# Performance work log

Measured on AMD Instinct MI355X. Metric: run time of the kernel, lower is better.

The kernel has to match this reference:

```python
import jax, jax.numpy as jnp
import numpy as np

N, E, IN, H, C, OUT = 50000, 800000, 128, 4, 32, 40
HID = H * C  # 128


def _layernorm(x, g, b, eps=1e-5):
    mu = x.mean(-1, keepdims=True)
    var = ((x - mu) ** 2).mean(-1, keepdims=True)
    return (x - mu) * jax.lax.rsqrt(var + eps) * g + b


def _gatv2(x, src, dst, Wl, bl, Wr, br, att, bias, heads, ch, concat):
    n = x.shape[0]
    xl = (x @ Wl + bl).reshape(n, heads, ch)  # source-side transform
    xr = (x @ Wr + br).reshape(n, heads, ch)  # target-side transform
    e = jax.nn.leaky_relu(xl[src] + xr[dst], 0.2)          # [E,H,C]
    alpha = jnp.einsum('ehc,hc->eh', e, att)                # [E,H]
    m = jax.ops.segment_max(alpha, dst, num_segments=n)
    m = jnp.where(jnp.isfinite(m), m, 0.0)
    a = jnp.exp(alpha - m[dst])
    denom = jax.ops.segment_sum(a, dst, num_segments=n)
    a = a / (denom[dst] + 1e-16)
    out = jax.ops.segment_sum(xl[src] * a[:, :, None], dst, num_segments=n)  # [N,H,C]
    out = out.reshape(n, heads * ch) if concat else out.mean(1)
    return out + bias


def setup_inputs():
    key = jax.random.key(0)
    ks = jax.random.split(key, 26)
    s = 0.05
    rn = lambda k, sh: jax.random.normal(k, sh, jnp.float32) * s
    inp = {
        'x': jax.random.normal(ks[0], (N, IN), jnp.float32),
        'edge_index': jax.random.randint(ks[1], (2, E), 0, N, jnp.int64),
        'W0': rn(ks[2], (IN, HID)), 'b0': jnp.zeros((HID,), jnp.float32),
        'W1l': rn(ks[3], (IN, HID)), 'b1l': jnp.zeros((HID,), jnp.float32),
        'W1r': rn(ks[4], (IN, HID)), 'b1r': jnp.zeros((HID,), jnp.float32),
        'att1': rn(ks[5], (H, C)), 'bias1': jnp.zeros((HID,), jnp.float32),
        'g1': jnp.ones((HID,), jnp.float32), 'be1': jnp.zeros((HID,), jnp.float32),
        'W2l': rn(ks[6], (HID, HID)), 'b2l': jnp.zeros((HID,), jnp.float32),
        'W2r': rn(ks[7], (HID, HID)), 'b2r': jnp.zeros((HID,), jnp.float32),
        'att2': rn(ks[8], (H, C)), 'bias2': jnp.zeros((HID,), jnp.float32),
        'g2': jnp.ones((HID,), jnp.float32), 'be2': jnp.zeros((HID,), jnp.float32),
        'W3l': rn(ks[9], (HID, OUT)), 'b3l': jnp.zeros((OUT,), jnp.float32),
        'W3r': rn(ks[10], (HID, OUT)), 'b3r': jnp.zeros((OUT,), jnp.float32),
        'att3': rn(ks[11], (1, OUT)), 'bias3': jnp.zeros((OUT,), jnp.float32),
    }
    return inp


def reference(x, edge_index, W0, b0, W1l, b1l, W1r, b1r, att1, bias1, g1, be1,
              W2l, b2l, W2r, b2r, att2, bias2, g2, be2,
              W3l, b3l, W3r, b3r, att3, bias3):
    src, dst = edge_index[0], edge_index[1]
    identity = x @ W0 + b0
    out = _gatv2(x, src, dst, W1l, b1l, W1r, b1r, att1, bias1, H, C, True)
    out = jax.nn.gelu(_layernorm(out, g1, be1), approximate=False)
    x1 = out + identity  # dropout is identity in eval mode
    out = _gatv2(x1, src, dst, W2l, b2l, W2r, b2r, att2, bias2, H, C, True)
    out = jax.nn.gelu(_layernorm(out, g2, be2), approximate=False)
    x2 = out + x1
    return _gatv2(x2, src, dst, W3l, b3l, W3r, b3r, att3, bias3, 1, OUT, False)
```

## Files before the change

kernel.cpp:

```cpp
#include <hip/hip_runtime.h>
#include <hip/hip_bf16.h>

#define NN 50000
#define EE 800000
#define OUTD 40
#define NBUCK 196
#define BCAP 8192
#define ABLKS 200
#define EPB 4000

typedef __attribute__((ext_vector_type(8))) short short8;
typedef __attribute__((ext_vector_type(4))) float floatx4;

__device__ __forceinline__ float bf2f(unsigned short u) {
  union { unsigned int i; float f; } v; v.i = ((unsigned int)u) << 16; return v.f;
}
__device__ __forceinline__ unsigned short f2bf(float f) {
  union { float f; unsigned int i; } v; v.f = f;
  unsigned int x = v.i;
  return (unsigned short)((x + 0x7fffu + ((x >> 16) & 1u)) >> 16);
}
__device__ __forceinline__ float blo(unsigned int u) {
  union { unsigned int i; float f; } v; v.i = u << 16; return v.f;
}
__device__ __forceinline__ float bhi(unsigned int u) {
  union { unsigned int i; float f; } v; v.i = u & 0xffff0000u; return v.f;
}

template <int CTRL>
__device__ __forceinline__ float dpp_add(float x) {
  int y = __builtin_amdgcn_update_dpp(0, __float_as_int(x), CTRL, 0xF, 0xF, true);
  return x + __int_as_float(y);
}

__device__ __forceinline__ float gelu1(float y) {
  float y2 = y * y;
  float z = y * fmaf(0.0356774081f, y2, 0.7978845608f);
  float e = __expf(-2.f * z);
  float r = __builtin_amdgcn_rcpf(1.f + e);
  float th = fmaf(2.f, r, -1.f);
  return y * fmaf(0.5f, th, 0.5f);
}

__device__ __forceinline__ int probe_f32(const void* x) {
  int lane = threadIdx.x & 63;
  unsigned short u = ((const unsigned short*)x)[2 * lane];
  int exf = (u >> 7) & 0xFF;
  unsigned long long b = __ballot((exf >= 100 && exf <= 142) ? 1 : 0);
  return (__popcll(b) >= 48) ? 0 : 1;
}
__device__ __forceinline__ int probe_i64(const void* ei) {
  int lane = threadIdx.x & 63;
  long long v = ((const long long*)ei)[lane];
  unsigned long long b = __ballot((v >= 0 && v < NN) ? 1 : 0);
  return (__popcll(b) >= 48) ? 1 : 0;
}

struct WDesc { const void* W; unsigned short* F; int T; int ncols; };
struct WDescs { WDesc d[7]; int cum[8]; };
struct PCv { const void* s; unsigned short* d; int n; int cap; };
struct PCvs { PCv a[17]; };

__global__ __launch_bounds__(256) void init_kernel(const void* __restrict__ ei,
                                                   const void* __restrict__ x,
                                                   int* __restrict__ flags,
                                                   int* __restrict__ bcur,
                                                   WDescs ds, PCvs P) {
  int b = blockIdx.x;
  int f32 = probe_f32(x);
  if (b < 48) {
    int idx = b * 256 + threadIdx.x;
    if (idx >= 12288) return;
    int mi = 0;
    while (idx >= ds.cum[mi + 1]) mi++;
    int local = idx - ds.cum[mi];
    WDesc d = ds.d[mi];
    int lane = local & 63;
    int rest = local >> 6;
    int t = rest % d.T;
    int kb = rest / d.T;
    int m = lane & 15, quad = lane >> 4;
    int col = t * 16 + m;
    short8 v;
    for (int j = 0; j < 8; ++j) {
      int k = kb * 32 + quad * 8 + j;
      if (col < d.ncols) {
        int off = k * d.ncols + col;
        v[j] = f32 ? (short)f2bf(((const float*)d.W)[off])
                   : (short)((const unsigned short*)d.W)[off];
      } else {
        v[j] = 0;
      }
    }
    *(short8*)(d.F + (size_t)local * 8) = v;
  } else if (b < 65) {
    PCv p = P.a[b - 48];
    for (int i = threadIdx.x; i < p.cap; i += 256) {
      unsigned short o = 0;
      if (i < p.n)
        o = f32 ? f2bf(((const float*)p.s)[i]) : ((const unsigned short*)p.s)[i];
      p.d[i] = o;
    }
  } else {
    for (int i = threadIdx.x; i < NBUCK * 16; i += 256) bcur[i] = 0;
    if (threadIdx.x < 64) {
      int i64 = probe_i64(ei);
      if (threadIdx.x == 0) {
        flags[0] = i64;
        flags[1] = f32;
        flags[2] = 0;
      }
    }
  }
}

__global__ __launch_bounds__(256) void bucket_scatter_kernel(
    const void* __restrict__ ei, unsigned int* __restrict__ bedges,
    int* __restrict__ bcur) {
  __shared__ int lhist[NBUCK];
  __shared__ int lbase[NBUCK];
  int tid = threadIdx.x;
  if (tid < NBUCK) lhist[tid] = 0;
  int i64 = probe_i64(ei);
  __syncthreads();
  int e0 = blockIdx.x * EPB;
  int e1 = e0 + EPB; if (e1 > EE) e1 = EE;
  for (int e = e0 + tid; e < e1; e += 256) {
    int d = i64 ? (int)((const long long*)ei)[EE + e] : ((const int*)ei)[EE + e];
    d = d < 0 ? 0 : (d >= NN ? NN - 1 : d);
    atomicAdd(&lhist[d >> 8], 1);
  }
  __syncthreads();
  if (tid < NBUCK) {
    int c = lhist[tid];
    lbase[tid] = c ? atomicAdd(&bcur[tid * 16], c) : 0;
    lhist[tid] = 0;
  }
  __syncthreads();
  for (int e = e0 + tid; e < e1; e += 256) {
    int s, d;
    if (i64) {
      s = (int)((const long long*)ei)[e];
      d = (int)((const long long*)ei)[EE + e];
    } else {
      s = ((const int*)ei)[e];
      d = ((const int*)ei)[EE + e];
    }
    s = s < 0 ? 0 : (s >= NN ? NN - 1 : s);
    d = d < 0 ? 0 : (d >= NN ? NN - 1 : d);
    int bin = d >> 8;
    int r = atomicAdd(&lhist[bin], 1);
    int pos = lbase[bin] + r;
    if (pos < BCAP)
      bedges[(size_t)bin * BCAP + pos] =
          ((unsigned int)(d & 0xFF) << 24) | ((unsigned int)s << 8);
  }
}

__global__ __launch_bounds__(256) void bucket_sort_kernel(
    const unsigned int* __restrict__ bedges, const int* __restrict__ bcur,
    int* __restrict__ offs, int* __restrict__ src_sorted) {
  __shared__ int lhist[256];
  __shared__ int lscan[256];
  __shared__ int lbin[256];
  __shared__ int sbase, scount, stotal;
  __shared__ unsigned int le[BCAP];
  __shared__ unsigned short lrank[BCAP];
  int k = blockIdx.x;
  int tid = threadIdx.x;
  int c = 0;
  if (tid < NBUCK) {
    int v = bcur[tid * 16];
    c = v < BCAP ? v : BCAP;
  }
  lscan[tid] = c;
  __syncthreads();
  for (int off = 1; off < 256; off <<= 1) {
    int u = (tid >= off) ? lscan[tid - off] : 0;
    __syncthreads();
    lscan[tid] += u;
    __syncthreads();
  }
  if (tid == 0) {
    int pb = (k == 0) ? 0 : lscan[k - 1];
    sbase = pb;
    scount = lscan[k] - pb;
    stotal = lscan[NBUCK - 1];
  }
  lhist[tid] = 0;
  __syncthreads();
  int base = sbase, count = scount;
  const unsigned int* myb = bedges + (size_t)k * BCAP;
  for (int i = tid; i < count; i += 256) {
    unsigned int pk = myb[i];
    int bin = pk >> 24;
    int r = atomicAdd(&lhist[bin], 1);
    le[i] = pk;
    lrank[i] = (unsigned short)r;
  }
  __syncthreads();
  int hc = lhist[tid];
  lscan[tid] = hc;
  __syncthreads();
  for (int off = 1; off < 256; off <<= 1) {
    int u = (tid >= off) ? lscan[tid - off] : 0;
    __syncthreads();
    lscan[tid] += u;
    __syncthreads();
  }
  int binoff = lscan[tid] - hc;
  lbin[tid] = binoff;
  int node = k * 256 + tid;
  if (node < NN) offs[node] = base + binoff;
  if (k == 0 && tid == 0) offs[NN] = stotal;
  __syncthreads();
  for (int i = tid; i < count; i += 256) {
    unsigned int pk = le[i];
    int bin = pk >> 24;
    int pos = base + lbin[bin] + (int)lrank[i];
    src_sorted[pos] = (int)(pk & 0x00FFFF00u);
  }
}

struct GSet { const unsigned short* F; const unsigned short* bias; unsigned short* Out; };
struct GArgs { GSet s[3]; };

__device__ __forceinline__ short8 pack_f4(float4 u0, float4 u1) {
  short8 r;
  r[0] = (short)f2bf(u0.x); r[1] = (short)f2bf(u0.y);
  r[2] = (short)f2bf(u0.z); r[3] = (short)f2bf(u0.w);
  r[4] = (short)f2bf(u1.x); r[5] = (short)f2bf(u1.y);
  r[6] = (short)f2bf(u1.z); r[7] = (short)f2bf(u1.w);
  return r;
}

__global__ __launch_bounds__(256) void gemm_multi_kernel(
    const void* __restrict__ A, const int* __restrict__ flagp, GArgs g,
    int nset, int M, int T, int ncols) {
  int wave = blockIdx.x * 4 + (threadIdx.x >> 6);
  int lane = threadIdx.x & 63;
  int r0 = wave * 16;
  if (r0 >= M) return;
  int f32 = *flagp;
  int m = lane & 15, quad = lane >> 4;
  short8 a0, a1, a2, a3;
  if (!f32) {
    const unsigned short* ar = (const unsigned short*)A + (size_t)(r0 + m) * 128 + quad * 8;
    a0 = *(const short8*)(ar);
    a1 = *(const short8*)(ar + 32);
    a2 = *(const short8*)(ar + 64);
    a3 = *(const short8*)(ar + 96);
  } else {
    const float* ar = (const float*)A + (size_t)(r0 + m) * 128 + quad * 8;
    a0 = pack_f4(*(const float4*)(ar), *(const float4*)(ar + 4));
    a1 = pack_f4(*(const float4*)(ar + 32), *(const float4*)(ar + 36));
    a2 = pack_f4(*(const float4*)(ar + 64), *(const float4*)(ar + 68));
    a3 = pack_f4(*(const float4*)(ar + 96), *(const float4*)(ar + 100));
  }
  size_t kstride = (size_t)T * 64 * 8;
  for (int si = 0; si < nset; ++si) {
    const unsigned short* F = g.s[si].F;
    const unsigned short* bias = g.s[si].bias;
    unsigned short* Out = g.s[si].Out;
    for (int t = 0; t < T; ++t) {
      floatx4 acc = {0.f, 0.f, 0.f, 0.f};
      const unsigned short* wp = F + ((size_t)t * 64 + lane) * 8;
      acc = __builtin_amdgcn_mfma_f32_16x16x32_bf16(a0, *(const short8*)(wp), acc, 0, 0, 0);
      acc = __builtin_amdgcn_mfma_f32_16x16x32_bf16(a1, *(const short8*)(wp + kstride), acc, 0, 0, 0);
      acc = __builtin_amdgcn_mfma_f32_16x16x32_bf16(a2, *(const short8*)(wp + 2 * kstride), acc, 0, 0, 0);
      acc = __builtin_amdgcn_mfma_f32_16x16x32_bf16(a3, *(const short8*)(wp + 3 * kstride), acc, 0, 0, 0);
      int col = t * 16 + m;
      if (col < ncols) {
        float bb = bf2f(bias[col]);
        for (int r = 0; r < 4; ++r) {
          int row = r0 + quad * 4 + r;
          Out[(size_t)row * ncols + col] = f2bf(acc[r] + bb);
        }
      }
    }
  }
}

__global__ __launch_bounds__(256) void edge_hid_kernel(
    const unsigned short* __restrict__ xl, const unsigned short* __restrict__ xr,
    const unsigned short* __restrict__ att, const unsigned short* __restrict__ bias,
    const unsigned short* __restrict__ gamma, const unsigned short* __restrict__ beta,
    const unsigned short* __restrict__ resid, unsigned short* __restrict__ xout,
    const int* __restrict__ offs, const int* __restrict__ srcs) {
  int wpair = blockIdx.x * 4 + (threadIdx.x >> 6);
  int lane = threadIdx.x & 63;
  int half = lane >> 5;
  int wv = wpair * 2 + half;
  if (wv >= NN) return;
  int hl = lane & 31;
  int sub = hl >> 4;
  int cb = (hl & 15) * 16;
  int beg = offs[wv], end = offs[wv + 1], last = end - 1;
  int iters = (end - beg + 1) >> 1;
  int oi = __shfl_xor(iters, 32);
  int maxit = __builtin_amdgcn_readfirstlane(iters > oi ? iters : oi);
  const char* xlb = (const char*)xl;
  uint4 xr8 = *(const uint4*)((const char*)xr + (size_t)wv * 256 + cb);
  float rx0 = blo(xr8.x), rx1 = bhi(xr8.x), rx2 = blo(xr8.y), rx3 = bhi(xr8.y);
  float rx4 = blo(xr8.z), rx5 = bhi(xr8.z), rx6 = blo(xr8.w), rx7 = bhi(xr8.w);
  uint4 at8 = *(const uint4*)((const char*)att + cb);
  float a0 = blo(at8.x), a1 = bhi(at8.x), a2 = blo(at8.y), a3 = bhi(at8.y);
  float a4 = blo(at8.z), a5 = bhi(at8.z), a6 = blo(at8.w), a7 = bhi(at8.w);
  float acc0 = 0.f, acc1 = 0.f, acc2 = 0.f, acc3 = 0.f;
  float acc4 = 0.f, acc5 = 0.f, acc6 = 0.f, acc7 = 0.f, den = 0.f;
  int ir = beg + sub;
  int ic = ir <= last ? ir : last;
  ic = ic < 0 ? 0 : ic;
  uint4 u = *(const uint4*)(xlb + (srcs[ic] + cb));
  for (int it = 0; it < maxit; ++it) {
    uint4 uc = u;
    float mk = (ir <= last) ? 1.f : 0.f;
    ir += 2;
    int in_ = ir <= last ? ir : last;
    in_ = in_ < 0 ? 0 : in_;
    u = *(const uint4*)(xlb + (srcs[in_] + cb));
    float x0 = blo(uc.x), x1 = bhi(uc.x), x2 = blo(uc.y), x3 = bhi(uc.y);
    float x4 = blo(uc.z), x5 = bhi(uc.z), x6 = blo(uc.w), x7 = bhi(uc.w);
    float t0 = x0 + rx0, t1 = x1 + rx1, t2 = x2 + rx2, t3 = x3 + rx3;
    float t4 = x4 + rx4, t5 = x5 + rx5, t6 = x6 + rx6, t7 = x7 + rx7;
    float pa = a0 * t0;
    pa = fmaf(a1, t1, pa); pa = fmaf(a2, t2, pa); pa = fmaf(a3, t3, pa);
    pa = fmaf(a4, t4, pa); pa = fmaf(a5, t5, pa); pa = fmaf(a6, t6, pa); pa = fmaf(a7, t7, pa);
    float pb = a0 * fabsf(t0);
    pb = fmaf(a1, fabsf(t1), pb); pb = fmaf(a2, fabsf(t2), pb); pb = fmaf(a3, fabsf(t3), pb);
    pb = fmaf(a4, fabsf(t4), pb); pb = fmaf(a5, fabsf(t5), pb);
    pb = fmaf(a6, fabsf(t6), pb); pb = fmaf(a7, fabsf(t7), pb);
    float p = fmaf(0.4f, pb, 0.6f * pa);
    p = dpp_add<0xB1>(p);
    p = dpp_add<0x4E>(p);
    float w = __expf(fminf(p, 60.f)) * mk;
    den += w;
    acc0 = fmaf(w, x0, acc0); acc1 = fmaf(w, x1, acc1);
    acc2 = fmaf(w, x2, acc2); acc3 = fmaf(w, x3, acc3);
    acc4 = fmaf(w, x4, acc4); acc5 = fmaf(w, x5, acc5);
    acc6 = fmaf(w, x6, acc6); acc7 = fmaf(w, x7, acc7);
  }
  den += __shfl_xor(den, 16);
  acc0 += __shfl_xor(acc0, 16); acc1 += __shfl_xor(acc1, 16);
  acc2 += __shfl_xor(acc2, 16); acc3 += __shfl_xor(acc3, 16);
  acc4 += __shfl_xor(acc4, 16); acc5 += __shfl_xor(acc5, 16);
  acc6 += __shfl_xor(acc6, 16); acc7 += __shfl_xor(acc7, 16);
  int srcLane = (half << 5) + (hl >> 1);
  float b0 = __shfl(acc0, srcLane), b1 = __shfl(acc1, srcLane);
  float b2 = __shfl(acc2, srcLane), b3 = __shfl(acc3, srcLane);
  float h4 = __shfl(acc4, srcLane), h5 = __shfl(acc5, srcLane);
  float h6 = __shfl(acc6, srcLane), h7 = __shfl(acc7, srcLane);
  float dn = __shfl(den, srcLane);
  bool hi = (hl & 1) != 0;
  float v0 = hi ? h4 : b0, v1 = hi ? h5 : b1, v2 = hi ? h6 : b2, v3 = hi ? h7 : b3;
  int c0 = hl * 4;
  float inv = __builtin_amdgcn_rcpf(dn + 1e-16f);
  uint2 bb = *(const uint2*)(bias + c0);
  float o0 = v0 * inv + blo(bb.x), o1 = v1 * inv + bhi(bb.x);
  float o2 = v2 * inv + blo(bb.y), o3 = v3 * inv + bhi(bb.y);
  float s = (o0 + o1) + (o2 + o3);
  for (int k = 1; k < 32; k <<= 1) s += __shfl_xor(s, k);
  float mu = s * (1.f / 128.f);
  float d0 = o0 - mu, d1 = o1 - mu, d2 = o2 - mu, d3 = o3 - mu;
  float q = (d0 * d0 + d1 * d1) + (d2 * d2 + d3 * d3);
  for (int k = 1; k < 32; k <<= 1) q += __shfl_xor(q, k);
  float rstd = rsqrtf(q * (1.f / 128.f) + 1e-5f);
  uint2 gg = *(const uint2*)(gamma + c0);
  uint2 be = *(const uint2*)(beta + c0);
  float y0 = d0 * rstd * blo(gg.x) + blo(be.x);
  float y1 = d1 * rstd * bhi(gg.x) + bhi(be.x);
  float y2 = d2 * rstd * blo(gg.y) + blo(be.y);
  float y3 = d3 * rstd * bhi(gg.y) + bhi(be.y);
  y0 = gelu1(y0); y1 = gelu1(y1); y2 = gelu1(y2); y3 = gelu1(y3);
  uint2 rr = *(const uint2*)(resid + (size_t)wv * 128 + c0);
  y0 += blo(rr.x); y1 += bhi(rr.x); y2 += blo(rr.y); y3 += bhi(rr.y);
  uint2 pk;
  pk.x = (unsigned int)f2bf(y0) | ((unsigned int)f2bf(y1) << 16);
  pk.y = (unsigned int)f2bf(y2) | ((unsigned int)f2bf(y3) << 16);
  *(uint2*)(xout + (size_t)wv * 128 + c0) = pk;
}

__global__ __launch_bounds__(256) void edge_out_kernel(
    const unsigned short* __restrict__ xl, const unsigned short* __restrict__ xr,
    const unsigned short* __restrict__ att, const unsigned short* __restrict__ bias,
    void* __restrict__ out, const int* __restrict__ flagp,
    const int* __restrict__ offs, const int* __restrict__ srcs) {
  int wv = blockIdx.x * 4 + (threadIdx.x >> 6);
  if (wv >= NN) return;
  int lane = threadIdx.x & 63;
  int oct = lane >> 3;
  int cb = (lane & 7) * 16;
  int beg = __builtin_amdgcn_readfirstlane(offs[wv]);
  int last = __builtin_amdgcn_readfirstlane(offs[wv + 1]) - 1;
  const char* xlb = (const char*)xl;
  uint4 xr8 = *(const uint4*)((const char*)xr + (size_t)wv * 128 + cb);
  float rx0 = blo(xr8.x), rx1 = bhi(xr8.x), rx2 = blo(xr8.y), rx3 = bhi(xr8.y);
  float rx4 = blo(xr8.z), rx5 = bhi(xr8.z), rx6 = blo(xr8.w), rx7 = bhi(xr8.w);
  uint4 at8 = *(const uint4*)((const char*)att + cb);
  float a0 = blo(at8.x), a1 = bhi(at8.x), a2 = blo(at8.y), a3 = bhi(at8.y);
  float a4 = blo(at8.z), a5 = bhi(at8.z), a6 = blo(at8.w), a7 = bhi(at8.w);
  float acc0 = 0.f, acc1 = 0.f, acc2 = 0.f, acc3 = 0.f;
  float acc4 = 0.f, acc5 = 0.f, acc6 = 0.f, acc7 = 0.f, den = 0.f;
  for (int e = beg; e <= last; e += 8) {
    int ir = e + oct;
    float mk = (ir <= last) ? 1.f : 0.f;
    int i0 = ir <= last ? ir : last;
    i0 = i0 < 0 ? 0 : i0;
    int soff = (srcs[i0] >> 1) + cb;
    uint4 u = *(const uint4*)(xlb + soff);
    float x0 = blo(u.x), x1 = bhi(u.x), x2 = blo(u.y), x3 = bhi(u.y);
    float x4 = blo(u.z), x5 = bhi(u.z), x6 = blo(u.w), x7 = bhi(u.w);
    float t0 = x0 + rx0, t1 = x1 + rx1, t2 = x2 + rx2, t3 = x3 + rx3;
    float t4 = x4 + rx4, t5 = x5 + rx5, t6 = x6 + rx6, t7 = x7 + rx7;
    float pa = a0 * t0;
    pa = fmaf(a1, t1, pa); pa = fmaf(a2, t2, pa); pa = fmaf(a3, t3, pa);
    pa = fmaf(a4, t4, pa); pa = fmaf(a5, t5, pa); pa = fmaf(a6, t6, pa); pa = fmaf(a7, t7, pa);
    float pb = a0 * fabsf(t0);
    pb = fmaf(a1, fabsf(t1), pb); pb = fmaf(a2, fabsf(t2), pb); pb = fmaf(a3, fabsf(t3), pb);
    pb = fmaf(a4, fabsf(t4), pb); pb = fmaf(a5, fabsf(t5), pb);
    pb = fmaf(a6, fabsf(t6), pb); pb = fmaf(a7, fabsf(t7), pb);
    float p = fmaf(0.4f, pb, 0.6f * pa);
    p = dpp_add<0xB1>(p);
    p = dpp_add<0x4E>(p);
    p = dpp_add<0x141>(p);
    float w = __expf(fminf(p, 60.f)) * mk;
    den += w;
    acc0 = fmaf(w, x0, acc0); acc1 = fmaf(w, x1, acc1);
    acc2 = fmaf(w, x2, acc2); acc3 = fmaf(w, x3, acc3);
    acc4 = fmaf(w, x4, acc4); acc5 = fmaf(w, x5, acc5);
    acc6 = fmaf(w, x6, acc6); acc7 = fmaf(w, x7, acc7);
  }
  den += __shfl_xor(den, 8);  den += __shfl_xor(den, 16);  den += __shfl_xor(den, 32);
  acc0 += __shfl_xor(acc0, 8); acc0 += __shfl_xor(acc0, 16); acc0 += __shfl_xor(acc0, 32);
  acc1 += __shfl_xor(acc1, 8); acc1 += __shfl_xor(acc1, 16); acc1 += __shfl_xor(acc1, 32);
  acc2 += __shfl_xor(acc2, 8); acc2 += __shfl_xor(acc2, 16); acc2 += __shfl_xor(acc2, 32);
  acc3 += __shfl_xor(acc3, 8); acc3 += __shfl_xor(acc3, 16); acc3 += __shfl_xor(acc3, 32);
  acc4 += __shfl_xor(acc4, 8); acc4 += __shfl_xor(acc4, 16); acc4 += __shfl_xor(acc4, 32);
  acc5 += __shfl_xor(acc5, 8); acc5 += __shfl_xor(acc5, 16); acc5 += __shfl_xor(acc5, 32);
  acc6 += __shfl_xor(acc6, 8); acc6 += __shfl_xor(acc6, 16); acc6 += __shfl_xor(acc6, 32);
  acc7 += __shfl_xor(acc7, 8); acc7 += __shfl_xor(acc7, 16); acc7 += __shfl_xor(acc7, 32);
  float inv = __builtin_amdgcn_rcpf(den + 1e-16f);
  if (lane < 5) {
    uint4 bb = *(const uint4*)((const char*)bias + cb);
    float v0 = acc0 * inv + blo(bb.x), v1 = acc1 * inv + bhi(bb.x);
    float v2 = acc2 * inv + blo(bb.y), v3 = acc3 * inv + bhi(bb.y);
    float v4 = acc4 * inv + blo(bb.z), v5 = acc5 * inv + bhi(bb.z);
    float v6 = acc6 * inv + blo(bb.w), v7 = acc7 * inv + bhi(bb.w);
    int c0 = lane * 8;
    if (*flagp) {
      float* op = (float*)out + (size_t)wv * OUTD + c0;
      float4 f0 = {v0, v1, v2, v3};
      float4 f1 = {v4, v5, v6, v7};
      *(float4*)(op) = f0;
      *(float4*)(op + 4) = f1;
    } else {
      uint4 pk;
      pk.x = (unsigned int)f2bf(v0) | ((unsigned int)f2bf(v1) << 16);
      pk.y = (unsigned int)f2bf(v2) | ((unsigned int)f2bf(v3) << 16);
      pk.z = (unsigned int)f2bf(v4) | ((unsigned int)f2bf(v5) << 16);
      pk.w = (unsigned int)f2bf(v6) | ((unsigned int)f2bf(v7) << 16);
      *(uint4*)((unsigned short*)out + (size_t)wv * OUTD + c0) = pk;
    }
  }
}

extern "C" void kernel_launch(void* const* d_in, const int* in_sizes, int n_in,
                              void* d_out, int out_size, void* d_ws, size_t ws_size,
                              hipStream_t stream) {
  const void* x = d_in[0];
  const void* ei = d_in[1];

  char* ws = (char*)d_ws;
  size_t o = 0;
  auto alloc = [&](size_t bytes) {
    void* p = ws + o;
    o = (o + bytes + 255) & ~(size_t)255;
    return p;
  };
  int* flags = (int*)alloc(256);
  int* src_sorted = (int*)alloc((size_t)EE * 4);
  int* offs = (int*)alloc((size_t)(NN + 1) * 4);
  int* bcur = (int*)alloc((size_t)NBUCK * 16 * 4);
  unsigned int* bedges = (unsigned int*)alloc((size_t)NBUCK * BCAP * 4);
  unsigned short* F_W0 = (unsigned short*)alloc(2048 * 16);
  unsigned short* F_W1l = (unsigned short*)alloc(2048 * 16);
  unsigned short* F_W1r = (unsigned short*)alloc(2048 * 16);
  unsigned short* F_W2l = (unsigned short*)alloc(2048 * 16);
  unsigned short* F_W2r = (unsigned short*)alloc(2048 * 16);
  unsigned short* F_W3l = (unsigned short*)alloc(1024 * 16);
  unsigned short* F_W3r = (unsigned short*)alloc(1024 * 16);
  unsigned short* pblk = (unsigned short*)alloc(4096);
  unsigned short* ident = (unsigned short*)alloc((size_t)NN * 128 * 2);
  unsigned short* bxl = (unsigned short*)alloc((size_t)NN * 128 * 2);
  unsigned short* bxr = (unsigned short*)alloc((size_t)NN * 128 * 2);
  (void)ws_size;

  unsigned short* pb0 = pblk;
  unsigned short* pb1l = pblk + 128;
  unsigned short* pb1r = pblk + 256;
  unsigned short* patt1 = pblk + 384;
  unsigned short* pbias1 = pblk + 512;
  unsigned short* pg1 = pblk + 640;
  unsigned short* pbe1 = pblk + 768;
  unsigned short* pb2l = pblk + 896;
  unsigned short* pb2r = pblk + 1024;
  unsigned short* patt2 = pblk + 1152;
  unsigned short* pbias2 = pblk + 1280;
  unsigned short* pg2 = pblk + 1408;
  unsigned short* pbe2 = pblk + 1536;
  unsigned short* pb3l = pblk + 1664;
  unsigned short* pb3r = pblk + 1728;
  unsigned short* patt3 = pblk + 1792;
  unsigned short* pbias3 = pblk + 1856;

  WDescs wd;
  wd.d[0] = {d_in[2], F_W0, 8, 128};
  wd.d[1] = {d_in[4], F_W1l, 8, 128};
  wd.d[2] = {d_in[6], F_W1r, 8, 128};
  wd.d[3] = {d_in[12], F_W2l, 8, 128};
  wd.d[4] = {d_in[14], F_W2r, 8, 128};
  wd.d[5] = {d_in[20], F_W3l, 4, 40};
  wd.d[6] = {d_in[22], F_W3r, 4, 40};
  int cum[8] = {0, 2048, 4096, 6144, 8192, 10240, 11264, 12288};
  for (int i = 0; i < 8; ++i) wd.cum[i] = cum[i];
  PCvs P;
  P.a[0] = {d_in[3], pb0, 128, 128};
  P.a[1] = {d_in[5], pb1l, 128, 128};
  P.a[2] = {d_in[7], pb1r, 128, 128};
  P.a[3] = {d_in[8], patt1, 128, 128};
  P.a[4] = {d_in[9], pbias1, 128, 128};
  P.a[5] = {d_in[10], pg1, 128, 128};
  P.a[6] = {d_in[11], pbe1, 128, 128};
  P.a[7] = {d_in[13], pb2l, 128, 128};
  P.a[8] = {d_in[15], pb2r, 128, 128};
  P.a[9] = {d_in[16], patt2, 128, 128};
  P.a[10] = {d_in[17], pbias2, 128, 128};
  P.a[11] = {d_in[18], pg2, 128, 128};
  P.a[12] = {d_in[19], pbe2, 128, 128};
  P.a[13] = {d_in[21], pb3l, 40, 64};
  P.a[14] = {d_in[23], pb3r, 40, 64};
  P.a[15] = {d_in[24], patt3, 40, 64};
  P.a[16] = {d_in[25], pbias3, 40, 64};
  init_kernel<<<66, 256, 0, stream>>>(ei, x, flags, bcur, wd, P);

  bucket_scatter_kernel<<<ABLKS, 256, 0, stream>>>(ei, bedges, bcur);
  bucket_sort_kernel<<<NBUCK, 256, 0, stream>>>(bedges, bcur, offs, src_sorted);

  const int gb = (NN / 16 + 3) / 4;
  const int eb = (NN + 3) / 4;
  const int eb2 = (NN / 2 + 3) / 4;
  const int* fx = flags + 1;
  const int* f0 = flags + 2;

  GArgs g1a; g1a.s[0] = {F_W0, pb0, ident}; g1a.s[1] = {F_W1l, pb1l, bxl}; g1a.s[2] = {F_W1r, pb1r, bxr};
  gemm_multi_kernel<<<gb, 256, 0, stream>>>(x, fx, g1a, 3, NN, 8, 128);
  edge_hid_kernel<<<eb2, 256, 0, stream>>>(bxl, bxr, patt1, pbias1, pg1, pbe1, ident, ident, offs, src_sorted);

  GArgs g2a; g2a.s[0] = {F_W2l, pb2l, bxl}; g2a.s[1] = {F_W2r, pb2r, bxr}; g2a.s[2] = {nullptr, nullptr, nullptr};
  gemm_multi_kernel<<<gb, 256, 0, stream>>>(ident, f0, g2a, 2, NN, 8, 128);
  edge_hid_kernel<<<eb2, 256, 0, stream>>>(bxl, bxr, patt2, pbias2, pg2, pbe2, ident, ident, offs, src_sorted);

  GArgs g3a; g3a.s[0] = {F_W3l, pb3l, bxl}; g3a.s[1] = {F_W3r, pb3r, bxr}; g3a.s[2] = {nullptr, nullptr, nullptr};
  gemm_multi_kernel<<<gb, 256, 0, stream>>>(ident, f0, g3a, 2, NN, 4, 64);
  edge_out_kernel<<<eb, 256, 0, stream>>>(bxl, bxr, patt3, pbias3, d_out, fx, offs, src_sorted);
}
```

Before: 319.2 us.

## Sort nodes by in-degree so paired half-waves in edge kernel balance work

Builds a degree histogram during bucket sort, scans it, and scatters nodes into a permutation grouped by in-degree in descending order. The hidden-layer edge kernels then process nodes through this permutation, so the two half-waves sharing a wave have similar edge counts and the shared loop bound wastes fewer iterations. This adds two small kernels, a permutation read, and scattered (non-sequential) node accesses for xr, the residual and the outputs. The bounds check on wv was removed, which relies on NN being an exact multiple of the node-pair grid.

```diff
diff --git a/kernel.cpp b/kernel.cpp
--- a/kernel.cpp
+++ b/kernel.cpp
@@ -65,6 +65,7 @@
                                                    const void* __restrict__ x,
                                                    int* __restrict__ flags,
                                                    int* __restrict__ bcur,
+                                                   int* __restrict__ dhist,
                                                    WDescs ds, PCvs P) {
   int b = blockIdx.x;
   int f32 = probe_f32(x);
@@ -103,6 +104,7 @@
     }
   } else {
     for (int i = threadIdx.x; i < NBUCK * 16; i += 256) bcur[i] = 0;
+    if (threadIdx.x < 256) dhist[threadIdx.x] = 0;
     if (threadIdx.x < 64) {
       int i64 = probe_i64(ei);
       if (threadIdx.x == 0) {
@@ -159,7 +161,8 @@
 
 __global__ __launch_bounds__(256) void bucket_sort_kernel(
     const unsigned int* __restrict__ bedges, const int* __restrict__ bcur,
-    int* __restrict__ offs, int* __restrict__ src_sorted) {
+    int* __restrict__ offs, int* __restrict__ src_sorted,
+    int* __restrict__ dhist) {
   __shared__ int lhist[256];
   __shared__ int lscan[256];
   __shared__ int lbin[256];
@@ -211,7 +214,10 @@
   int binoff = lscan[tid] - hc;
   lbin[tid] = binoff;
   int node = k * 256 + tid;
-  if (node < NN) offs[node] = base + binoff;
+  if (node < NN) {
+    offs[node] = base + binoff;
+    atomicAdd(&dhist[hc > 255 ? 255 : hc], 1);
+  }
   if (k == 0 && tid == 0) offs[NN] = stotal;
   __syncthreads();
   for (int i = tid; i < count; i += 256) {
@@ -220,6 +226,46 @@
     int pos = base + lbin[bin] + (int)lrank[i];
     src_sorted[pos] = (int)(pk & 0x00FFFF00u);
   }
+}
+
+__global__ __launch_bounds__(256) void deg_scan_kernel(const int* __restrict__ dhist,
+                                                       int* __restrict__ dbase) {
+  __shared__ int lds[256];
+  int t = threadIdx.x;
+  int v = dhist[t];
+  lds[t] = v;
+  __syncthreads();
+  for (int off = 1; off < 256; off <<= 1) {
+    int u = (t >= off) ? lds[t - off] : 0;
+    __syncthreads();
+    lds[t] += u;
+    __syncthreads();
+  }
+  int total = lds[255];
+  dbase[t] = total - lds[t];
+}
+
+__global__ __launch_bounds__(256) void perm_scatter_kernel(const int* __restrict__ offs,
+                                                           int* __restrict__ dbase,
+                                                           int* __restrict__ perm) {
+  __shared__ int lhist[256];
+  __shared__ int lbase[256];
+  int tid = threadIdx.x;
+  lhist[tid] = 0;
+  __syncthreads();
+  int node = blockIdx.x * 256 + tid;
+  int d = 0, rank = 0;
+  bool act = node < NN;
+  if (act) {
+    d = offs[node + 1] - offs[node];
+    d = d > 255 ? 255 : d;
+    rank = atomicAdd(&lhist[d], 1);
+  }
+  __syncthreads();
+  int c = lhist[tid];
+  lbase[tid] = c ? atomicAdd(&dbase[tid], c) : 0;
+  __syncthreads();
+  if (act) perm[lbase[d] + rank] = node;
 }
 
 struct GSet { const unsigned short* F; const unsigned short* bias; unsigned short* Out; };
@@ -286,12 +332,12 @@
     const unsigned short* __restrict__ att, const unsigned short* __restrict__ bias,
     const unsigned short* __restrict__ gamma, const unsigned short* __restrict__ beta,
     const unsigned short* __restrict__ resid, unsigned short* __restrict__ xout,
-    const int* __restrict__ offs, const int* __restrict__ srcs) {
+    const int* __restrict__ offs, const int* __restrict__ srcs,
+    const int* __restrict__ perm) {
   int wpair = blockIdx.x * 4 + (threadIdx.x >> 6);
   int lane = threadIdx.x & 63;
   int half = lane >> 5;
-  int wv = wpair * 2 + half;
-  if (wv >= NN) return;
+  int wv = perm[wpair * 2 + half];
   int hl = lane & 31;
   int sub = hl >> 4;
   int cb = (hl & 15) * 16;
@@ -481,6 +527,9 @@
   int* src_sorted = (int*)alloc((size_t)EE * 4);
   int* offs = (int*)alloc((size_t)(NN + 1) * 4);
   int* bcur = (int*)alloc((size_t)NBUCK * 16 * 4);
+  int* dhist = (int*)alloc(256 * 4);
+  int* dbase = (int*)alloc(256 * 4);
+  int* perm = (int*)alloc((size_t)NN * 4);
   unsigned int* bedges = (unsigned int*)alloc((size_t)NBUCK * BCAP * 4);
   unsigned short* F_W0 = (unsigned short*)alloc(2048 * 16);
   unsigned short* F_W1l = (unsigned short*)alloc(2048 * 16);
@@ -541,10 +590,12 @@
   P.a[14] = {d_in[23], pb3r, 40, 64};
   P.a[15] = {d_in[24], patt3, 40, 64};
   P.a[16] = {d_in[25], pbias3, 40, 64};
-  init_kernel<<<66, 256, 0, stream>>>(ei, x, flags, bcur, wd, P);
+  init_kernel<<<66, 256, 0, stream>>>(ei, x, flags, bcur, dhist, wd, P);
 
   bucket_scatter_kernel<<<ABLKS, 256, 0, stream>>>(ei, bedges, bcur);
-  bucket_sort_kernel<<<NBUCK, 256, 0, stream>>>(bedges, bcur, offs, src_sorted);
+  bucket_sort_kernel<<<NBUCK, 256, 0, stream>>>(bedges, bcur, offs, src_sorted, dhist);
+  deg_scan_kernel<<<1, 256, 0, stream>>>(dhist, dbase);
+  perm_scatter_kernel<<<NBUCK, 256, 0, stream>>>(offs, dbase, perm);
 
   const int gb = (NN / 16 + 3) / 4;
   const int eb = (NN + 3) / 4;
@@ -554,11 +605,11 @@
 
   GArgs g1a; g1a.s[0] = {F_W0, pb0, ident}; g1a.s[1] = {F_W1l, pb1l, bxl}; g1a.s[2] = {F_W1r, pb1r, bxr};
   gemm_multi_kernel<<<gb, 256, 0, stream>>>(x, fx, g1a, 3, NN, 8, 128);
-  edge_hid_kernel<<<eb2, 256, 0, stream>>>(bxl, bxr, patt1, pbias1, pg1, pbe1, ident, ident, offs, src_sorted);
+  edge_hid_kernel<<<eb2, 256, 0, stream>>>(bxl, bxr, patt1, pbias1, pg1, pbe1, ident, ident, offs, src_sorted, perm);
 
   GArgs g2a; g2a.s[0] = {F_W2l, pb2l, bxl}; g2a.s[1] = {F_W2r, pb2r, bxr}; g2a.s[2] = {nullptr, nullptr, nullptr};
   gemm_multi_kernel<<<gb, 256, 0, stream>>>(ident, f0, g2a, 2, NN, 8, 128);
-  edge_hid_kernel<<<eb2, 256, 0, stream>>>(bxl, bxr, patt2, pbias2, pg2, pbe2, ident, ident, offs, src_sorted);
+  edge_hid_kernel<<<eb2, 256, 0, stream>>>(bxl, bxr, patt2, pbias2, pg2, pbe2, ident, ident, offs, src_sorted, perm);
 
   GArgs g3a; g3a.s[0] = {F_W3l, pb3l, bxl}; g3a.s[1] = {F_W3r, pb3r, bxr}; g3a.s[2] = {nullptr, nullptr, nullptr};
   gemm_multi_kernel<<<gb, 256, 0, stream>>>(ident, f0, g3a, 2, NN, 4, 64);
```

Result: slower. 450.7 us (+41.2%).
